# Performance work log

Measured on AMD Instinct MI355X. Metric: run time of the kernel, lower is better.

Reference implementation:

```python
import jax, jax.numpy as jnp
import numpy as np

WS = 7          # window size (fixed: last_idx=169=(2*7-1)^2)
NP = 1          # num_priorset
NH = 8          # num heads
DIM = 256
SHIFT = 3
N = WS * WS     # 49 tokens per window
NK = N + 3 * NP # 52 K/V tokens (window + uk/fg/bg priors)


def _rel_index():
    coords = np.stack(np.meshgrid(np.arange(WS), np.arange(WS), indexing='ij')).reshape(2, -1)
    rel = (coords[:, :, None] - coords[:, None, :]).transpose(1, 2, 0).astype(np.int64)
    rel[:, :, 0] += WS - 1
    rel[:, :, 1] += WS - 1
    rel[:, :, 0] *= 2 * WS - 1
    idx = rel.sum(-1)                      # (49,49) in [0,168]
    full = np.full((N, NK), 169, dtype=np.int64)
    full[:, :N] = idx
    for j in range(3 * NP):
        full[:, N + j] = 169 + j           # dedicated bias rows for priors
    return jnp.asarray(full)

REL_IDX = _rel_index()


def _ln(t, g, b, eps=1e-5):
    mu = t.mean(-1, keepdims=True)
    var = ((t - mu) ** 2).mean(-1, keepdims=True)
    return (t - mu) * jax.lax.rsqrt(var + eps) * g + b


def setup_inputs() -> dict:
    key = jax.random.key(0)
    ks = jax.random.split(key, 16)
    B, H, W, C = 4, 112, 112, DIM
    nW = (H // WS) * (W // WS)
    hid = 4 * C
    inp = {
        'x': jax.random.normal(ks[0], (B, H * W, C), jnp.float32),
        'mask_matrix': jax.random.normal(ks[1], (nW, N, N), jnp.float32),
        'area_fg': jax.random.uniform(ks[2], (B, H, W, 1), jnp.float32),
        'area_bg': jax.random.uniform(ks[3], (B, H, W, 1), jnp.float32),
        'area_uk': jax.random.uniform(ks[4], (B, H, W, 1), jnp.float32),
        'norm1_g': jnp.ones((C,), jnp.float32),
        'norm1_b': jnp.zeros((C,), jnp.float32),
        'norm2_g': jnp.ones((C,), jnp.float32),
        'norm2_b': jnp.zeros((C,), jnp.float32),
        'qkv_w': jax.random.normal(ks[5], (3 * C, C), jnp.float32) * 0.02,
        'qkv_b': jnp.zeros((3 * C,), jnp.float32),
        'proj_w': jax.random.normal(ks[6], (C, C), jnp.float32) * 0.02,
        'proj_b': jnp.zeros((C,), jnp.float32),
        'rel_table': jax.random.normal(ks[7], (169 + 3 * NP, NH), jnp.float32) * 0.02,
        'fc1_w': jax.random.normal(ks[8], (hid, C), jnp.float32) * 0.02,
        'fc1_b': jnp.zeros((hid,), jnp.float32),
        'fc2_w': jax.random.normal(ks[9], (C, hid), jnp.float32) * 0.02,
        'fc2_b': jnp.zeros((C,), jnp.float32),
        'H': 112,
        'W': 112,
    }
    return inp


def reference(x, mask_matrix, area_fg, area_bg, area_uk,
              norm1_g, norm1_b, norm2_g, norm2_b,
              qkv_w, qkv_b, proj_w, proj_b, rel_table,
              fc1_w, fc1_b, fc2_w, fc2_b, H, W):
    B, L, C = x.shape
    d = C // NH
    scale = d ** -0.5
    nWh, nWw = H // WS, W // WS
    nW = nWh * nWw

    shortcut = x
    x4 = x.reshape(B, H, W, C)
    eps = 1e-9
    # masked global-average prior tokens (B, C)
    def pooled(area):
        return (area * x4).sum((1, 2)) / (area.sum((1, 2)) + eps)
    uk, fg, bg = pooled(area_uk), pooled(area_fg), pooled(area_bg)

    xn = _ln(x, norm1_g, norm1_b).reshape(B, H, W, C)
    uk_n = _ln(uk, norm1_g, norm1_b)
    fg_n = _ln(fg, norm1_g, norm1_b)
    bg_n = _ln(bg, norm1_g, norm1_b)

    # cyclic shift + window partition (H,W divisible by WS -> no padding)
    xs = jnp.roll(xn, (-SHIFT, -SHIFT), (1, 2))
    xw = xs.reshape(B, nWh, WS, nWw, WS, C).transpose(0, 1, 3, 2, 4, 5).reshape(B * nW, N, C)

    # prior highway tokens (order: unknown, fg, bg) and per-window copies
    ph = jnp.stack([uk_n, fg_n, bg_n], axis=1)                      # (B,3,C)
    pr = jnp.broadcast_to(ph[:, None], (B, nW, 3, C)).reshape(B * nW, 3, C)
    xk = jnp.concatenate([xw, pr], axis=1)                          # (B_,52,C)

    qkv = (xk @ qkv_w.T + qkv_b).reshape(B * nW, NK, 3, NH, d)
    q = qkv[:, :N, 0].transpose(0, 2, 1, 3) * scale                 # (B_,h,49,d)
    k = qkv[:, :, 1].transpose(0, 2, 1, 3)                          # (B_,h,52,d)
    v = qkv[:, :, 2].transpose(0, 2, 1, 3)

    attn = jnp.einsum('bhnd,bhmd->bhnm', q, k)                      # (B_,h,49,52)
    bias = rel_table[REL_IDX].transpose(2, 0, 1)                    # (h,49,52)
    attn = attn + bias[None]
    mask = jnp.pad(mask_matrix, ((0, 0), (0, 0), (0, 3 * NP)))      # (nW,49,52)
    attn = attn.reshape(B, nW, NH, N, NK) + mask[None, :, None]
    attn = jax.nn.softmax(attn.reshape(B * nW, NH, N, NK), axis=-1)

    out = jnp.einsum('bhnm,bhmd->bhnd', attn, v)
    out = out.transpose(0, 2, 1, 3).reshape(B * nW, N, C)
    out = out @ proj_w.T + proj_b

    # prior highway: qkv on priors, keep V, project
    ph_qkv = (ph @ qkv_w.T + qkv_b).reshape(B, 3 * NP, 3, NH, d)
    v_hw = ph_qkv[:, :, 2].reshape(B, 3 * NP, C) @ proj_w.T + proj_b

    # window reverse + reverse shift
    xo = out.reshape(B, nWh, nWw, WS, WS, C).transpose(0, 1, 3, 2, 4, 5).reshape(B, H, W, C)
    xo = jnp.roll(xo, (SHIFT, SHIFT), (1, 2)).reshape(B, L, C)

    x = shortcut + xo
    h = _ln(x, norm2_g, norm2_b)
    h = jax.nn.gelu(h @ fc1_w.T + fc1_b, approximate=False)
    x = x + (h @ fc2_w.T + fc2_b)
    return x, v_hw
```

## Files before the change

### kernel.cpp

```cpp
#include <hip/hip_runtime.h>
#include <hip/hip_bf16.h>
#include <math.h>

typedef __bf16 bf16;
typedef bf16 bf16x8 __attribute__((ext_vector_type(8)));
typedef bf16 bf16x4 __attribute__((ext_vector_type(4)));
typedef float f32x4 __attribute__((ext_vector_type(4)));

constexpr int DIM   = 256;
constexpr int NH    = 8;
constexpr int LTOT  = 112 * 112;
constexpr int BTOT  = 4;
constexpr int MROWS = BTOT * LTOT;
constexpr int MQKV  = MROWS + BTOT * 3;
constexpr int NTOK  = 49;
constexpr int NKV   = 52;

__global__ void cvt_f32_bf16(const float* __restrict__ s, bf16* __restrict__ d, int n) {
    int i = blockIdx.x * 256 + threadIdx.x;
    if (i < n) d[i] = (bf16)s[i];
}

__global__ __launch_bounds__(256) void pool_partial(
    const float* __restrict__ x, const float* __restrict__ afg,
    const float* __restrict__ abg, const float* __restrict__ auk,
    float* __restrict__ pnum, float* __restrict__ pden)
{
    int b = blockIdx.x / 49, ch = blockIdx.x % 49;
    int p0 = ch * 256, tid = threadIdx.x;
    __shared__ float su[256], sf[256], sb[256];
    int p = p0 + tid;
    su[tid] = auk[b * LTOT + p];
    sf[tid] = afg[b * LTOT + p];
    sb[tid] = abg[b * LTOT + p];
    __syncthreads();
    float nu = 0.f, nf = 0.f, nb = 0.f;
    const float* xp = x + ((size_t)b * LTOT + p0) * DIM + tid;
    for (int pp = 0; pp < 256; ++pp) {
        float xv = xp[(size_t)pp * DIM];
        nu += su[pp] * xv; nf += sf[pp] * xv; nb += sb[pp] * xv;
    }
    size_t base = (size_t)blockIdx.x * 3 * DIM + tid;
    pnum[base]           = nu;
    pnum[base + DIM]     = nf;
    pnum[base + 2 * DIM] = nb;
    if (tid < 3) {
        const float* sptr = tid == 0 ? su : (tid == 1 ? sf : sb);
        float t = 0.f;
        for (int i = 0; i < 256; ++i) t += sptr[i];
        pden[blockIdx.x * 3 + tid] = t;
    }
}

__device__ __forceinline__ void block_meanvar(float v, float& mu, float& rstd, float eps) {
    float s = v, s2 = v * v;
    #pragma unroll
    for (int o = 32; o >= 1; o >>= 1) { s += __shfl_down(s, o); s2 += __shfl_down(s2, o); }
    __shared__ float ps[4], ps2[4];
    int w = threadIdx.x >> 6, ln = threadIdx.x & 63;
    if (ln == 0) { ps[w] = s; ps2[w] = s2; }
    __syncthreads();
    float S  = ps[0] + ps[1] + ps[2] + ps[3];
    float S2 = ps2[0] + ps2[1] + ps2[2] + ps2[3];
    mu = S * (1.f / 256.f);
    float var = S2 * (1.f / 256.f) - mu * mu;
    rstd = rsqrtf(var + eps);
}

__global__ __launch_bounds__(256) void prior_ln(
    const float* __restrict__ pnum, const float* __restrict__ pden,
    const float* __restrict__ g, const float* __restrict__ bt, bf16* __restrict__ xn)
{
    int b = blockIdx.x / 3, j = blockIdx.x % 3, tid = threadIdx.x;
    float s = 0.f, den = 0.f;
    for (int ch = 0; ch < 49; ++ch) {
        s   += pnum[((size_t)(b * 49 + ch) * 3 + j) * DIM + tid];
        den += pden[(b * 49 + ch) * 3 + j];
    }
    float v = s / (den + 1e-9f);
    float mu, rs;
    block_meanvar(v, mu, rs, 1e-5f);
    xn[((size_t)MROWS + blockIdx.x) * DIM + tid] = (bf16)((v - mu) * rs * g[tid] + bt[tid]);
}

__global__ __launch_bounds__(256) void ln1_kernel(
    const float* __restrict__ x, const float* __restrict__ g,
    const float* __restrict__ bt, bf16* __restrict__ xn)
{
    size_t row = blockIdx.x; int tid = threadIdx.x;
    float v = x[row * DIM + tid];
    float mu, rs;
    block_meanvar(v, mu, rs, 1e-5f);
    xn[row * DIM + tid] = (bf16)((v - mu) * rs * g[tid] + bt[tid]);
}

__device__ __forceinline__ void load_lds16(const void* g, void* l) {
    __builtin_amdgcn_global_load_lds((const __attribute__((address_space(1))) void*)g,
                                     (__attribute__((address_space(3))) void*)l, 16, 0, 0);
}

template <int EPI>
__global__ __launch_bounds__(256) void gemm_bt(
    const bf16* __restrict__ A, const bf16* __restrict__ W,
    const float* __restrict__ bias, bf16* __restrict__ Cb,
    float* __restrict__ Cf, const float* __restrict__ resid,
    int M, int N, int K)
{
    __shared__ __align__(16) char smem[49152];
    const int tid = threadIdx.x;
    const int wv = tid >> 6, lane = tid & 63;

    const int gx = gridDim.x;
    const int nwg = gx * (int)gridDim.y;
    int lin = blockIdx.y * gx + blockIdx.x;
    int xcd = lin & 7, loc = lin >> 3;
    int qq = nwg >> 3, rr = nwg & 7;
    int nid = (xcd < rr ? xcd * (qq + 1) : rr * (qq + 1) + (xcd - rr) * qq) + loc;
    int by = nid / gx, bx = nid - by * gx;
    const int m0 = by * 128, n0 = bx * 128;

    const int r  = tid >> 2;
    const int kb = (((tid & 3) ^ ((tid >> 3) & 3)) * 8);
    const int wr = (wv >> 1) * 64, wc = (wv & 1) * 64;
    const int fr = lane & 15;
    const int fo = (((lane >> 4) ^ ((fr >> 1) & 3)) * 8);

    int ra0 = m0 + r;      if (ra0 >= M) ra0 = M - 1;
    int ra1 = m0 + r + 64; if (ra1 >= M) ra1 = M - 1;
    const bf16* pA0 = A + (size_t)ra0 * K + kb;
    const bf16* pA1 = A + (size_t)ra1 * K + kb;
    const bf16* pW0 = W + (size_t)(n0 + r) * K + kb;
    const bf16* pW1 = W + (size_t)(n0 + r + 64) * K + kb;

    const f32x4 zero = {0.f, 0.f, 0.f, 0.f};
    f32x4 acc[4][4];
    #pragma unroll
    for (int i = 0; i < 4; ++i)
        #pragma unroll
        for (int j = 0; j < 4; ++j) acc[i][j] = zero;

    const int nK = K >> 5;

    auto stage = [&](int kt, int b) {
        bf16* Ab = (bf16*)(smem + b * 16384);
        bf16* Bb = (bf16*)(smem + b * 16384 + 8192);
        const int off = kt * 32;
        load_lds16(pA0 + off, Ab + wv * 512);
        load_lds16(pA1 + off, Ab + 2048 + wv * 512);
        load_lds16(pW0 + off, Bb + wv * 512);
        load_lds16(pW1 + off, Bb + 2048 + wv * 512);
    };

    stage(0, 0);
    stage(1, 1);

    int cur = 0;
    for (int kt = 0; kt < nK; ++kt) {
        asm volatile("s_waitcnt lgkmcnt(0)" ::: "memory");
        if (kt < nK - 1) asm volatile("s_waitcnt vmcnt(4)" ::: "memory");
        else             asm volatile("s_waitcnt vmcnt(0)" ::: "memory");
        __builtin_amdgcn_s_barrier();
        if (kt + 2 < nK) {
            int nb = cur + 2; if (nb >= 3) nb -= 3;
            stage(kt + 2, nb);
        }
        const bf16* Ac = (const bf16*)(smem + cur * 16384);
        const bf16* Bc = (const bf16*)(smem + cur * 16384 + 8192);
        bf16x8 af[4], bw[4];
        #pragma unroll
        for (int i = 0; i < 4; ++i) af[i] = *(const bf16x8*)(Ac + (wr + i * 16 + fr) * 32 + fo);
        #pragma unroll
        for (int i = 0; i < 4; ++i) bw[i] = *(const bf16x8*)(Bc + (wc + i * 16 + fr) * 32 + fo);
        #pragma unroll
        for (int i = 0; i < 4; ++i)
            #pragma unroll
            for (int j = 0; j < 4; ++j)
                acc[i][j] = __builtin_amdgcn_mfma_f32_16x16x32_bf16(af[i], bw[j], acc[i][j], 0, 0, 0);
        ++cur; if (cur == 3) cur = 0;
    }
    __syncthreads();

    const int cr = (lane >> 4) * 4, cc = lane & 15;
    if constexpr (EPI == 3) {
        float* Cs = (float*)smem;
        #pragma unroll
        for (int half = 0; half < 2; ++half) {
            if (wr == half * 64) {
                #pragma unroll
                for (int i = 0; i < 4; ++i)
                    #pragma unroll
                    for (int j = 0; j < 4; ++j) {
                        const int col = wc + j * 16 + cc;
                        const float bv = bias[n0 + col];
                        #pragma unroll
                        for (int q = 0; q < 4; ++q)
                            Cs[(i * 16 + cr + q) * 132 + col] = acc[i][j][q] + bv;
                    }
            }
            __syncthreads();
            for (int p = tid; p < 2048; p += 256) {
                const int row = p >> 5, seg = (p & 31) * 4;
                const int gr = m0 + half * 64 + row;
                if (gr < M) {
                    f32x4 v = *(const f32x4*)(Cs + row * 132 + seg);
                    const size_t o = (size_t)gr * N + n0 + seg;
                    f32x4 rv = *(const f32x4*)(resid + o);
                    *(f32x4*)(Cf + o) = v + rv;
                }
            }
            __syncthreads();
        }
    } else {
        bf16* Csb = (bf16*)smem;
        #pragma unroll
        for (int i = 0; i < 4; ++i)
            #pragma unroll
            for (int j = 0; j < 4; ++j) {
                const int col = wc + j * 16 + cc;
                const float bv = bias[n0 + col];
                #pragma unroll
                for (int q = 0; q < 4; ++q) {
                    float v = acc[i][j][q] + bv;
                    if constexpr (EPI == 2) {
                        float u = 0.7978845608028654f * (v + 0.044715f * v * v * v);
                        v = v / (1.f + __expf(-2.f * u));
                    }
                    Csb[(wr + i * 16 + cr + q) * 144 + col] = (bf16)v;
                }
            }
        __syncthreads();
        for (int p = tid; p < 2048; p += 256) {
            const int row = p >> 4, seg = (p & 15) * 8;
            const int gr = m0 + row;
            if (gr < M)
                *(bf16x8*)(Cb + (size_t)gr * N + n0 + seg) = *(const bf16x8*)(Csb + row * 144 + seg);
        }
    }
}

__global__ __launch_bounds__(256) void proj_ln2(
    const bf16* __restrict__ A, const bf16* __restrict__ W,
    const float* __restrict__ bias, const float* __restrict__ x,
    const float* __restrict__ g, const float* __restrict__ bt,
    float* __restrict__ x2, bf16* __restrict__ ln2)
{
    __shared__ __align__(16) char smem[40960];
    bf16* As = (bf16*)smem;
    bf16* Bs = (bf16*)(smem + 8192);

    const int tid = threadIdx.x;
    const int wv = tid >> 6, lane = tid & 63;
    const int m0 = blockIdx.x * 64;

    const int r4 = tid >> 2;
    const int kb = (((tid & 3) ^ ((tid >> 3) & 3)) * 8);
    const int fr = lane & 15;
    const int fo = (((lane >> 4) ^ ((fr >> 1) & 3)) * 8);

    const bf16* pA  = A + (size_t)(m0 + r4) * 256 + kb;
    const bf16* pW0 = W + (size_t)(r4)       * 256 + kb;
    const bf16* pW1 = W + (size_t)(r4 + 64)  * 256 + kb;
    const bf16* pW2 = W + (size_t)(r4 + 128) * 256 + kb;
    const bf16* pW3 = W + (size_t)(r4 + 192) * 256 + kb;

    const f32x4 zero = {0.f, 0.f, 0.f, 0.f};
    f32x4 acc[4][4];
    #pragma unroll
    for (int i = 0; i < 4; ++i)
        #pragma unroll
        for (int j = 0; j < 4; ++j) acc[i][j] = zero;

    auto stage = [&](int kt, int b) {
        const int off = kt * 32;
        load_lds16(pA  + off, As + b * 2048 + wv * 512);
        load_lds16(pW0 + off, Bs + b * 8192 + wv * 512);
        load_lds16(pW1 + off, Bs + b * 8192 + 2048 + wv * 512);
        load_lds16(pW2 + off, Bs + b * 8192 + 4096 + wv * 512);
        load_lds16(pW3 + off, Bs + b * 8192 + 6144 + wv * 512);
    };

    stage(0, 0);
    __syncthreads();
    int cur = 0;
    for (int kt = 0; kt < 8; ++kt) {
        if (kt + 1 < 8) stage(kt + 1, cur ^ 1);
        const bf16* Ac = As + cur * 2048;
        const bf16* Bc = Bs + cur * 8192;
        bf16x8 af[4], bw[4];
        #pragma unroll
        for (int i = 0; i < 4; ++i) af[i] = *(const bf16x8*)(Ac + (i * 16 + fr) * 32 + fo);
        #pragma unroll
        for (int j = 0; j < 4; ++j) bw[j] = *(const bf16x8*)(Bc + (wv * 64 + j * 16 + fr) * 32 + fo);
        #pragma unroll
        for (int i = 0; i < 4; ++i)
            #pragma unroll
            for (int j = 0; j < 4; ++j)
                acc[i][j] = __builtin_amdgcn_mfma_f32_16x16x32_bf16(af[i], bw[j], acc[i][j], 0, 0, 0);
        __syncthreads();
        cur ^= 1;
    }

    float* red = (float*)smem;
    const int cr = (lane >> 4) * 4, cc = lane & 15;

    int nrw[4][4];
    #pragma unroll
    for (int i = 0; i < 4; ++i)
        #pragma unroll
        for (int q = 0; q < 4; ++q) {
            int ar = m0 + i * 16 + cr + q;
            int bwin = ar / 49;
            int n = ar - bwin * 49;
            int bb = bwin >> 8, w = bwin & 255;
            int ni = n / 7, nj = n - ni * 7;
            int hh = (w >> 4) * 7 + ni + 3;  if (hh >= 112) hh -= 112;
            int ww2 = (w & 15) * 7 + nj + 3; if (ww2 >= 112) ww2 -= 112;
            nrw[i][q] = bb * LTOT + hh * 112 + ww2;
        }

    float s1[4][4], s2[4][4];
    #pragma unroll
    for (int i = 0; i < 4; ++i)
        #pragma unroll
        for (int q = 0; q < 4; ++q) { s1[i][q] = 0.f; s2[i][q] = 0.f; }

    #pragma unroll
    for (int j = 0; j < 4; ++j) {
        const int col = wv * 64 + j * 16 + cc;
        const float bv = bias[col];
        #pragma unroll
        for (int i = 0; i < 4; ++i)
            #pragma unroll
            for (int q = 0; q < 4; ++q) {
                float v = acc[i][j][q] + bv + x[(size_t)nrw[i][q] * 256 + col];
                acc[i][j][q] = v;
                s1[i][q] += v; s2[i][q] += v * v;
            }
    }
    #pragma unroll
    for (int o = 1; o < 16; o <<= 1)
        #pragma unroll
        for (int i = 0; i < 4; ++i)
            #pragma unroll
            for (int q = 0; q < 4; ++q) {
                s1[i][q] += __shfl_xor(s1[i][q], o);
                s2[i][q] += __shfl_xor(s2[i][q], o);
            }
    if (cc == 0) {
        #pragma unroll
        for (int i = 0; i < 4; ++i)
            #pragma unroll
            for (int q = 0; q < 4; ++q) {
                int m = i * 16 + cr + q;
                red[m * 8 + wv * 2]     = s1[i][q];
                red[m * 8 + wv * 2 + 1] = s2[i][q];
            }
    }
    __syncthreads();

    float mu[4][4], rs[4][4];
    #pragma unroll
    for (int i = 0; i < 4; ++i)
        #pragma unroll
        for (int q = 0; q < 4; ++q) {
            int m = i * 16 + cr + q;
            float S  = red[m * 8] + red[m * 8 + 2] + red[m * 8 + 4] + red[m * 8 + 6];
            float S2 = red[m * 8 + 1] + red[m * 8 + 3] + red[m * 8 + 5] + red[m * 8 + 7];
            float mm = S * (1.f / 256.f);
            float var = S2 * (1.f / 256.f) - mm * mm;
            mu[i][q] = mm;
            rs[i][q] = rsqrtf(var + 1e-5f);
        }
    #pragma unroll
    for (int j = 0; j < 4; ++j) {
        const int col = wv * 64 + j * 16 + cc;
        const float gv = g[col], bv2 = bt[col];
        #pragma unroll
        for (int i = 0; i < 4; ++i)
            #pragma unroll
            for (int q = 0; q < 4; ++q) {
                float v = acc[i][j][q];
                size_t o = (size_t)nrw[i][q] * 256 + col;
                x2[o] = v;
                ln2[o] = (bf16)((v - mu[i][q]) * rs[i][q] * gv + bv2);
            }
    }
}

__global__ __launch_bounds__(512, 1) void attn_kernel(
    const bf16* __restrict__ qkv, const float* __restrict__ mask,
    const float* __restrict__ rel, bf16* __restrict__ att_out)
{
    __shared__ int rowtab[52];
    __shared__ float mLds[64 * 67];
    __shared__ float rLds[1376];
    __shared__ __align__(16) bf16 vT[8 * 32 * 80];
    __shared__ __align__(16) bf16 pbuf[8 * 64 * 80];

    const int tid = threadIdx.x;
    const int bw = blockIdx.x;
    const int b = bw >> 8, w = bw & 255;
    const int wh = w >> 4, wwi = w & 15;

    if (tid < 52) {
        int row;
        if (tid < 49) {
            int i = tid / 7, j = tid % 7;
            int gh = wh * 7 + i + 3;  if (gh >= 112) gh -= 112;
            int gw = wwi * 7 + j + 3; if (gw >= 112) gw -= 112;
            row = b * LTOT + gh * 112 + gw;
        } else {
            row = MROWS + b * 3 + (tid - 49);
        }
        rowtab[tid] = row;
    }
    __syncthreads();

    for (int e = tid; e < 64 * 67; e += 512) {
        int q = e / 67, k = e % 67;
        mLds[e] = (q < 49 && k < 49) ? mask[(size_t)w * 2401 + q * 49 + k] : 0.f;
    }
    for (int e = tid; e < 1376; e += 512) rLds[e] = rel[e];
    for (int e = tid; e < 256 * 12; e += 512) {
        int rr = e / 12, c = 52 + e % 12;
        vT[rr * 80 + c] = (bf16)0.f;
    }
    for (int e = tid; e < 52 * 256; e += 512) {
        int key = e >> 8, c = e & 255;
        vT[c * 80 + key] = qkv[(size_t)rowtab[key] * 768 + 512 + c];
    }
    __syncthreads();

    const int h    = tid >> 6;
    const int lane = tid & 63;
    const int cl   = lane & 15;
    const int hi4  = lane >> 4;
    const int cr   = hi4 * 4;
    const int fo   = hi4 * 8;

    bf16x8 kf[4], qf[4];
    #pragma unroll
    for (int i = 0; i < 4; ++i) {
        int key = 16 * i + cl; if (key > 51) key = 51;
        kf[i] = *(const bf16x8*)(qkv + (size_t)rowtab[key] * 768 + 256 + h * 32 + fo);
    }
    #pragma unroll
    for (int j = 0; j < 4; ++j) {
        int qq = 16 * j + cl; if (qq > 48) qq = 48;
        qf[j] = *(const bf16x8*)(qkv + (size_t)rowtab[qq] * 768 + h * 32 + fo);
    }
    const f32x4 zero = {0.f, 0.f, 0.f, 0.f};
    f32x4 acc[4][4];
    #pragma unroll
    for (int i = 0; i < 4; ++i)
        #pragma unroll
        for (int j = 0; j < 4; ++j) acc[i][j] = zero;
    #pragma unroll
    for (int i = 0; i < 4; ++i)
        #pragma unroll
        for (int j = 0; j < 4; ++j)
            acc[i][j] = __builtin_amdgcn_mfma_f32_16x16x32_bf16(kf[i], qf[j], acc[i][j], 0, 0, 0);

    int kb[4][4];
    #pragma unroll
    for (int i = 0; i < 4; ++i)
        #pragma unroll
        for (int r = 0; r < 4; ++r) {
            int key = 16 * i + cr + r;
            kb[i][r] = (key / 7) * 13 + (key % 7);
        }
    bf16* pW = pbuf + h * (64 * 80);
    #pragma unroll
    for (int j = 0; j < 4; ++j) {
        const int q = 16 * j + cl;
        const int i1 = q / 7, j1 = q % 7;
        const int qb = (i1 + 6) * 13 + (j1 + 6);
        float sv[16];
        float mx = -3e38f;
        #pragma unroll
        for (int i = 0; i < 4; ++i)
            #pragma unroll
            for (int r = 0; r < 4; ++r) {
                int key = 16 * i + cr + r;
                int idx = key < 49 ? (qb - kb[i][r]) : (169 + key - 49);
                idx = idx < 0 ? 0 : (idx > 171 ? 171 : idx);
                float s = acc[i][j][r] * 0.17677669529663687f
                        + mLds[q * 67 + key] + rLds[idx * 8 + h];
                if (key >= 52) s = -3e38f;
                sv[i * 4 + r] = s;
                mx = fmaxf(mx, s);
            }
        mx = fmaxf(mx, __shfl_xor(mx, 16));
        mx = fmaxf(mx, __shfl_xor(mx, 32));
        float sum = 0.f;
        #pragma unroll
        for (int e = 0; e < 16; ++e) { float p = __expf(sv[e] - mx); sv[e] = p; sum += p; }
        sum += __shfl_xor(sum, 16);
        sum += __shfl_xor(sum, 32);
        const float inv = 1.f / sum;
        #pragma unroll
        for (int i = 0; i < 4; ++i) {
            bf16x4 pk;
            #pragma unroll
            for (int r = 0; r < 4; ++r) pk[r] = (bf16)(sv[i * 4 + r] * inv);
            *(bf16x4*)(pW + q * 80 + 16 * i + cr) = pk;
        }
    }

    f32x4 oacc[4][2];
    #pragma unroll
    for (int i = 0; i < 4; ++i) { oacc[i][0] = zero; oacc[i][1] = zero; }
    #pragma unroll
    for (int ks = 0; ks < 2; ++ks) {
        bf16x8 vf[2];
        #pragma unroll
        for (int j2 = 0; j2 < 2; ++j2)
            vf[j2] = *(const bf16x8*)(vT + (h * 32 + 16 * j2 + cl) * 80 + 32 * ks + fo);
        #pragma unroll
        for (int i = 0; i < 4; ++i) {
            bf16x8 pf = *(const bf16x8*)(pW + (16 * i + cl) * 80 + 32 * ks + fo);
            #pragma unroll
            for (int j2 = 0; j2 < 2; ++j2)
                oacc[i][j2] = __builtin_amdgcn_mfma_f32_16x16x32_bf16(pf, vf[j2], oacc[i][j2], 0, 0, 0);
        }
    }

    #pragma unroll
    for (int i = 0; i < 4; ++i)
        #pragma unroll
        for (int r = 0; r < 4; ++r) {
            int q = 16 * i + cr + r;
            if (q < 49) {
                bf16* op = att_out + ((size_t)bw * 49 + q) * 256 + h * 32 + cl;
                op[0]  = (bf16)oacc[i][0][r];
                op[16] = (bf16)oacc[i][1][r];
            }
        }
}

__global__ __launch_bounds__(256) void vhw_kernel(
    const bf16* __restrict__ qkv, const float* __restrict__ pw,
    const float* __restrict__ pb, float* __restrict__ outp)
{
    int rowI = blockIdx.x;
    int c = threadIdx.x;
    const bf16* vp = qkv + (size_t)(MROWS + rowI) * 768 + 512;
    const float* wr_ = pw + (size_t)c * DIM;
    float acc = pb[c];
    for (int k = 0; k < DIM; ++k) acc += (float)vp[k] * wr_[k];
    outp[(size_t)rowI * DIM + c] = acc;
}

extern "C" void kernel_launch(void* const* d_in, const int* in_sizes, int n_in,
                              void* d_out, int out_size, void* d_ws, size_t ws_size,
                              hipStream_t stream)
{
    const float* x     = (const float*)d_in[0];
    const float* mask  = (const float*)d_in[1];
    const float* afg   = (const float*)d_in[2];
    const float* abg   = (const float*)d_in[3];
    const float* auk   = (const float*)d_in[4];
    const float* n1g   = (const float*)d_in[5];
    const float* n1b   = (const float*)d_in[6];
    const float* n2g   = (const float*)d_in[7];
    const float* n2b   = (const float*)d_in[8];
    const float* qkvw  = (const float*)d_in[9];
    const float* qkvb  = (const float*)d_in[10];
    const float* projw = (const float*)d_in[11];
    const float* projb = (const float*)d_in[12];
    const float* rel   = (const float*)d_in[13];
    const float* fc1w  = (const float*)d_in[14];
    const float* fc1b  = (const float*)d_in[15];
    const float* fc2w  = (const float*)d_in[16];
    const float* fc2b  = (const float*)d_in[17];
    float* out = (float*)d_out;
    char*  ws  = (char*)d_ws;

    bf16*  wq   = (bf16*)(ws + 0);
    bf16*  wp   = (bf16*)(ws + 393216);
    bf16*  wf1  = (bf16*)(ws + 524288);
    bf16*  wf2  = (bf16*)(ws + 1048576);
    float* pnum = (float*)(ws + 1572864);
    float* pden = (float*)(ws + 1572864 + 602112);
    bf16* xn    = (bf16*)(ws + (2ull << 20));
    bf16* atto  = (bf16*)(ws + (2ull << 20));
    bf16* hbuf  = (bf16*)(ws + (2ull << 20));
    bf16* qkvo  = (bf16*)(ws + (28ull << 20));
    bf16* ln2b  = (bf16*)(ws + (102ull << 20));

    cvt_f32_bf16<<<(196608 + 255) / 256, 256, 0, stream>>>(qkvw, wq, 196608);
    cvt_f32_bf16<<<(65536  + 255) / 256, 256, 0, stream>>>(projw, wp, 65536);
    cvt_f32_bf16<<<(262144 + 255) / 256, 256, 0, stream>>>(fc1w, wf1, 262144);
    cvt_f32_bf16<<<(262144 + 255) / 256, 256, 0, stream>>>(fc2w, wf2, 262144);

    pool_partial<<<BTOT * 49, 256, 0, stream>>>(x, afg, abg, auk, pnum, pden);
    prior_ln<<<12, 256, 0, stream>>>(pnum, pden, n1g, n1b, xn);
    ln1_kernel<<<MROWS, 256, 0, stream>>>(x, n1g, n1b, xn);

    gemm_bt<0><<<dim3(6, 393), 256, 0, stream>>>(xn, wq, qkvb, qkvo, nullptr, nullptr, MQKV, 768, 256);

    attn_kernel<<<BTOT * 256, 512, 0, stream>>>(qkvo, mask, rel, atto);
    vhw_kernel<<<12, 256, 0, stream>>>(qkvo, projw, projb, out + (size_t)MROWS * DIM);

    proj_ln2<<<MROWS / 64, 256, 0, stream>>>(atto, wp, projb, x, n2g, n2b, out, ln2b);

    gemm_bt<2><<<dim3(8, 392), 256, 0, stream>>>(ln2b, wf1, fc1b, hbuf, nullptr, nullptr, MROWS, 1024, 256);
    gemm_bt<3><<<dim3(2, 392), 256, 0, stream>>>(hbuf, wf2, fc2b, nullptr, out, out, MROWS, 256, 1024);

    (void)in_sizes; (void)n_in; (void)out_size; (void)ws_size;
}
```

Before: 328.4 us.

## Add K=256 GEMM keeping whole weight tile in LDS for QKV and fc1

```diff
diff --git a/kernel.cpp b/kernel.cpp
--- a/kernel.cpp
+++ b/kernel.cpp
@@ -97,6 +97,97 @@
 __device__ __forceinline__ void load_lds16(const void* g, void* l) {
     __builtin_amdgcn_global_load_lds((const __attribute__((address_space(1))) void*)g,
                                      (__attribute__((address_space(3))) void*)l, 16, 0, 0);
+}
+
+template <int EPI, int K>
+__global__ __launch_bounds__(256, 4) void gemm_bs(
+    const bf16* __restrict__ A, const bf16* __restrict__ W,
+    const float* __restrict__ bias, bf16* __restrict__ C,
+    int M, int N)
+{
+    constexpr int NK = K / 32;
+    __shared__ __align__(16) char smem[36864];
+    bf16* Wl = (bf16*)smem;
+
+    const int tid = threadIdx.x;
+    const int wv = tid >> 6, lane = tid & 63;
+
+    const int gx = gridDim.x;
+    const int nwg = gx * (int)gridDim.y;
+    int lin = blockIdx.y * gx + blockIdx.x;
+    int xcd = lin & 7, loc = lin >> 3;
+    int qq = nwg >> 3, rr = nwg & 7;
+    int nid = (xcd < rr ? xcd * (qq + 1) : rr * (qq + 1) + (xcd - rr) * qq) + loc;
+    int by = nid / gx, bx = nid - by * gx;
+    const int m0 = by * 256, n0 = bx * 64;
+
+    const int r4 = tid >> 2;
+    const int kbs = (((tid & 3) ^ ((tid >> 3) & 3)) * 8);
+    const bf16* pW = W + (size_t)(n0 + r4) * K + kbs;
+    #pragma unroll
+    for (int kt = 0; kt < NK; ++kt)
+        load_lds16(pW + kt * 32, Wl + kt * 2048 + wv * 512);
+    __syncthreads();
+
+    const int fr = lane & 15, hi4 = lane >> 4;
+    const int fo = (hi4 ^ ((fr >> 1) & 3)) * 8;
+
+    const bf16* pA[4];
+    #pragma unroll
+    for (int i = 0; i < 4; ++i) {
+        int rowi = m0 + wv * 64 + i * 16 + fr;
+        if (rowi >= M) rowi = M - 1;
+        pA[i] = A + (size_t)rowi * K + hi4 * 8;
+    }
+
+    const f32x4 zero = {0.f, 0.f, 0.f, 0.f};
+    f32x4 acc[4][4];
+    #pragma unroll
+    for (int i = 0; i < 4; ++i)
+        #pragma unroll
+        for (int j = 0; j < 4; ++j) acc[i][j] = zero;
+
+    #pragma unroll
+    for (int kt = 0; kt < NK; ++kt) {
+        bf16x8 af[4], bw[4];
+        #pragma unroll
+        for (int i = 0; i < 4; ++i) af[i] = *(const bf16x8*)(pA[i] + kt * 32);
+        #pragma unroll
+        for (int j = 0; j < 4; ++j) bw[j] = *(const bf16x8*)(Wl + kt * 2048 + (j * 16 + fr) * 32 + fo);
+        #pragma unroll
+        for (int i = 0; i < 4; ++i)
+            #pragma unroll
+            for (int j = 0; j < 4; ++j)
+                acc[i][j] = __builtin_amdgcn_mfma_f32_16x16x32_bf16(af[i], bw[j], acc[i][j], 0, 0, 0);
+    }
+    __syncthreads();
+
+    bf16* stg = (bf16*)smem + wv * (64 * 72);
+    const int cr = hi4 * 4;
+    #pragma unroll
+    for (int i = 0; i < 4; ++i)
+        #pragma unroll
+        for (int j = 0; j < 4; ++j) {
+            const int col = j * 16 + fr;
+            const float bv = bias[n0 + col];
+            #pragma unroll
+            for (int q = 0; q < 4; ++q) {
+                float v = acc[i][j][q] + bv;
+                if constexpr (EPI == 2) {
+                    float u = 0.7978845608028654f * (v + 0.044715f * v * v * v);
+                    v = v / (1.f + __expf(-2.f * u));
+                }
+                stg[(i * 16 + cr + q) * 72 + col] = (bf16)v;
+            }
+        }
+    #pragma unroll
+    for (int s = 0; s < 8; ++s) {
+        const int row = s * 8 + (lane >> 3);
+        const int seg = (lane & 7) * 8;
+        const int grow = m0 + wv * 64 + row;
+        if (grow < M)
+            *(bf16x8*)(C + (size_t)grow * N + n0 + seg) = *(const bf16x8*)(stg + row * 72 + seg);
+    }
 }
 
 template <int EPI>
@@ -597,14 +688,15 @@
     prior_ln<<<12, 256, 0, stream>>>(pnum, pden, n1g, n1b, xn);
     ln1_kernel<<<MROWS, 256, 0, stream>>>(x, n1g, n1b, xn);
 
-    gemm_bt<0><<<dim3(6, 393), 256, 0, stream>>>(xn, wq, qkvb, qkvo, nullptr, nullptr, MQKV, 768, 256);
+    gemm_bs<0, 256><<<dim3(12, 197), 256, 0, stream>>>(xn, wq, qkvb, qkvo, MQKV, 768);
 
     attn_kernel<<<BTOT * 256, 512, 0, stream>>>(qkvo, mask, rel, atto);
     vhw_kernel<<<12, 256, 0, stream>>>(qkvo, projw, projb, out + (size_t)MROWS * DIM);
 
     proj_ln2<<<MROWS / 64, 256, 0, stream>>>(atto, wp, projb, x, n2g, n2b, out, ln2b);
 
-    gemm_bt<2><<<dim3(8, 392), 256, 0, stream>>>(ln2b, wf1, fc1b, hbuf, nullptr, nullptr, MROWS, 1024, 256);
+    gemm_bs<2, 256><<<dim3(16, 196), 256, 0, stream>>>(ln2b, wf1, fc1b, hbuf, MROWS, 1024);
+
     gemm_bt<3><<<dim3(2, 392), 256, 0, stream>>>(hbuf, wf2, fc2b, nullptr, out, out, MROWS, 256, 1024);
 
     (void)in_sizes; (void)n_in; (void)out_size; (void)ws_size;
```

After: 355.4 us. +8.2%, slower.
